# Performance work log

Hardware: AMD Instinct MI355X
Metric: run time of the kernel (lower is better)

The kernel has to match this reference:

```python
import jax, jax.numpy as jnp
import numpy as np

B, F, U, A, H = 8192, 1024, 256, 16, 8  # batch, in_features, units_layer, num_actions, hidden(=8)


def _coagent_layer(x, W0, b0, W1, b1, W2, b2):
    # x: [B, f_in]; stacked weights for U independent tiny MLPs (grouped GEMMs)
    h = jax.nn.relu(jnp.einsum('bf,uhf->buh', x, W0) + b0)   # [B, U, H]
    h = jax.nn.relu(jnp.einsum('buh,ugh->bug', h, W1) + b1)  # [B, U, H]
    q = jnp.einsum('bug,uag->bua', h, W2) + b2               # [B, U, A]
    # greedy action per coagent (epsilon-greedy with greedy=True / epsilon=0)
    return jnp.argmax(q, axis=-1).astype(jnp.float32)        # [B, U]


def setup_inputs() -> dict:
    key = jax.random.key(0)
    ks = jax.random.split(key, 19)
    n = lambda k, shape, fan: (jax.random.normal(k, shape, dtype=jnp.float32)
                               / jnp.sqrt(jnp.float32(fan)))
    return {
        'state': jax.random.normal(ks[0], (B, F), dtype=jnp.float32),
        # coagent layer 0: in_features -> 8 -> 8 -> A, stacked over U units
        'W0_0': n(ks[1], (U, H, F), F), 'b0_0': jnp.zeros((U, H), jnp.float32),
        'W1_0': n(ks[2], (U, H, H), H), 'b1_0': jnp.zeros((U, H), jnp.float32),
        'W2_0': n(ks[3], (U, A, H), H), 'b2_0': jnp.zeros((U, A), jnp.float32),
        # coagent layer 1: units_layer -> 8 -> 8 -> A, stacked over U units
        'W0_1': n(ks[4], (U, H, U), U), 'b0_1': jnp.zeros((U, H), jnp.float32),
        'W1_1': n(ks[5], (U, H, H), H), 'b1_1': jnp.zeros((U, H), jnp.float32),
        'W2_1': n(ks[6], (U, A, H), H), 'b2_1': jnp.zeros((U, A), jnp.float32),
        # Policy head: units_layer -> 8 -> 8 -> 1
        'PW0': n(ks[7], (H, U), U), 'Pb0': jnp.zeros((H,), jnp.float32),
        'PW1': n(ks[8], (H, H), H), 'Pb1': jnp.zeros((H,), jnp.float32),
        'PW2': n(ks[9], (1, H), H), 'Pb2': jnp.zeros((1,), jnp.float32),
    }


def reference(state, W0_0, b0_0, W1_0, b1_0, W2_0, b2_0,
              W0_1, b0_1, W1_1, b1_1, W2_1, b2_1,
              PW0, Pb0, PW1, Pb1, PW2, Pb2):
    a0 = _coagent_layer(state, W0_0, b0_0, W1_0, b1_0, W2_0, b2_0)  # [B, U]
    a1 = _coagent_layer(a0, W0_1, b0_1, W1_1, b1_1, W2_1, b2_1)     # [B, U]
    h = jax.nn.relu(a1 @ PW0.T + Pb0)
    h = jax.nn.relu(h @ PW1.T + Pb1)
    return h @ PW2.T + Pb2  # [B, 1]
```

## Files before the change

### kernel.cpp

```cpp
#include <hip/hip_runtime.h>
#include <cstring>
#include <cstdint>

#define B_TOTAL 8192
#define F_IN    1024
#define U_UNITS 256
#define NACT    16
#define HID     8

typedef float    f32x4  __attribute__((ext_vector_type(4)));
typedef _Float16 half8  __attribute__((ext_vector_type(8)));


__device__ __forceinline__ void gload_lds16(const _Float16* g, _Float16* l)
{
    __builtin_amdgcn_global_load_lds(
        (const __attribute__((address_space(1))) void*)g,
        (__attribute__((address_space(3))) void*)l,
        16, 0, 0);
}

__global__ __launch_bounds__(256)
void pack3_kernel(const float* __restrict__ s0, _Float16* __restrict__ d0h, _Float16* __restrict__ d0l,
                  const float* __restrict__ s1, _Float16* __restrict__ d1h, _Float16* __restrict__ d1l,
                  const float* __restrict__ s2, _Float16* __restrict__ d2h, _Float16* __restrict__ d2l)
{
    constexpr int NB0 = (B_TOTAL / 16) * (F_IN / 128);
    constexpr int NB1 = (U_UNITS * HID / 16) * (F_IN / 128);
    __shared__ float ls[16 * 132];
    int b = blockIdx.x;
    const float* src; _Float16 *dh, *dl; int K, lg;
    if (b < NB0)            { src = s0; dh = d0h; dl = d0l; K = F_IN;    lg = 3; }
    else if (b < NB0 + NB1) { b -= NB0; src = s1; dh = d1h; dl = d1l; K = F_IN; lg = 3; }
    else                    { b -= NB0 + NB1; src = s2; dh = d2h; dl = d2l; K = U_UNITS; lg = 1; }

    const int tid = threadIdx.x;
    const int mt  = b >> lg;
    const int kb  = b & ((1 << lg) - 1);
    const int r0  = mt * 16;

#pragma unroll
    for (int i = 0; i < 2; ++i) {
        const int e = tid + (i << 8);
        const int row = e >> 5;
        const int c4  = e & 31;
        f32x4 v = *reinterpret_cast<const f32x4*>(
            &src[(size_t)(r0 + row) * K + (kb << 7) + (c4 << 2)]);
        *reinterpret_cast<f32x4*>(&ls[row * 132 + (c4 << 2)]) = v;
    }
    __syncthreads();

    const int k8 = tid >> 4, r = tid & 15;
    float x[8];
#pragma unroll
    for (int j = 0; j < 8; ++j) x[j] = ls[r * 132 + (k8 << 3) + j];
    half8 h, l;
#pragma unroll
    for (int j = 0; j < 8; ++j) {
        h[j] = (_Float16)x[j];
        l[j] = (_Float16)((x[j] - (float)h[j]) * 2048.0f);
    }
    const size_t off = (((size_t)mt * (K >> 5)) + (kb << 2) + (k8 >> 2)) * 512
                     + (size_t)(((k8 & 3) << 4) + r) * 8;
    *reinterpret_cast<half8*>(&dh[off]) = h;
    *reinterpret_cast<half8*>(&dl[off]) = l;
}

constexpr int BM = 128, BN = 64;

template<int K_TOTAL, bool A_SPLIT, bool OUT_TF32>
__global__ __launch_bounds__(256, 4)
void coagent_mfma(const _Float16* __restrict__ Ahg, const _Float16* __restrict__ Alg,
                  const _Float16* __restrict__ Bhg, const _Float16* __restrict__ Blg,
                  const float* __restrict__ b0, const float* __restrict__ W1,
                  const float* __restrict__ b1, const float* __restrict__ W2,
                  const float* __restrict__ b2, void* __restrict__ outp)
{
    constexpr int BUFH  = A_SPLIT ? 12288 : 8192;
    constexpr int BOFFH = A_SPLIT ? 8192 : 4096;
    constexpr int BOFFL = A_SPLIT ? 10240 : 6144;
    constexpr int NCH   = A_SPLIT ? 6 : 4;

    struct EpiBufs { float Hs[BM][BN + 1]; _Float16 ab[BM * 8]; };
    union SMemU { _Float16 stage[2][BUFH]; EpiBufs epi; };
    __shared__ SMemU sm;

    constexpr int NTK = K_TOTAL >> 5;
    constexpr size_t TS = (size_t)NTK * 512;

    const int tid  = threadIdx.x;
    const int wave = tid >> 6;
    const int lane = tid & 63;
    const int quad = lane >> 4;
    const int l15  = lane & 15;

    const int flat = blockIdx.y * gridDim.x + blockIdx.x;
    const int xcd  = flat & 7;
    const int j    = flat >> 3;
    const int m0   = ((xcd << 3) | (j >> 5)) * BM;
    const int n0   = (j & 31) * BN;

    const int wmi = wave >> 1, wni = wave & 1;
    const int at  = wmi * 4;
    const int bt  = wni * 2;
    const int wm  = wmi * 64, wn = wni * 32;

    const int wave_u = __builtin_amdgcn_readfirstlane(wave);
    const _Float16* gs[NCH];
#pragma unroll
    for (int i = 0; i < NCH; ++i) {
        const int c = wave_u * NCH + i;
        const _Float16* base; int tile;
        if (A_SPLIT) {
            if (c < 8)       { base = Ahg; tile = (m0 >> 4) + c; }
            else if (c < 16) { base = Alg; tile = (m0 >> 4) + (c - 8); }
            else if (c < 20) { base = Bhg; tile = (n0 >> 4) + (c - 16); }
            else             { base = Blg; tile = (n0 >> 4) + (c - 20); }
        } else {
            if (c < 8)       { base = Ahg; tile = (m0 >> 4) + c; }
            else if (c < 12) { base = Bhg; tile = (n0 >> 4) + (c - 8); }
            else             { base = Blg; tile = (n0 >> 4) + (c - 12); }
        }
        gs[i] = base + (size_t)tile * TS;
    }
    const int loff = lane * 8;

    f32x4 acc1[4][2];
    f32x4 acc2[4][2];
#pragma unroll
    for (int i = 0; i < 4; ++i)
#pragma unroll
        for (int jj = 0; jj < 2; ++jj) { acc1[i][jj] = {0.f,0.f,0.f,0.f}; acc2[i][jj] = {0.f,0.f,0.f,0.f}; }

#pragma unroll
    for (int i = 0; i < NCH; ++i)
        gload_lds16(gs[i] + loff, &sm.stage[0][(wave_u * NCH + i) * 512]);
    __syncthreads();

    int cur = 0;
#pragma unroll 1
    for (int kt = 0; kt < NTK; ++kt) {
        if (kt + 1 < NTK) {
            _Float16* nb = &sm.stage[cur ^ 1][0];
#pragma unroll
            for (int i = 0; i < NCH; ++i)
                gload_lds16(gs[i] + (size_t)(kt + 1) * 512 + loff,
                            nb + (wave_u * NCH + i) * 512);
        }

        const _Float16* sb = &sm.stage[cur][0];
        half8 af[4], la[4];
#pragma unroll
        for (int mt = 0; mt < 4; ++mt)
            af[mt] = *reinterpret_cast<const half8*>(&sb[(at + mt) * 512 + lane * 8]);
        if constexpr (A_SPLIT) {
#pragma unroll
            for (int mt = 0; mt < 4; ++mt)
                la[mt] = *reinterpret_cast<const half8*>(&sb[4096 + (at + mt) * 512 + lane * 8]);
        }

#pragma unroll
        for (int nt = 0; nt < 2; ++nt) {
            half8 bf = *reinterpret_cast<const half8*>(&sb[BOFFH + (bt + nt) * 512 + lane * 8]);
            half8 lb = *reinterpret_cast<const half8*>(&sb[BOFFL + (bt + nt) * 512 + lane * 8]);
#pragma unroll
            for (int mt = 0; mt < 4; ++mt)
                acc1[mt][nt] = __builtin_amdgcn_mfma_f32_16x16x32_f16(af[mt], bf, acc1[mt][nt], 0, 0, 0);
            if constexpr (A_SPLIT) {
#pragma unroll
                for (int mt = 0; mt < 4; ++mt)
                    acc2[mt][nt] = __builtin_amdgcn_mfma_f32_16x16x32_f16(la[mt], bf, acc2[mt][nt], 0, 0, 0);
            }
#pragma unroll
            for (int mt = 0; mt < 4; ++mt)
                acc2[mt][nt] = __builtin_amdgcn_mfma_f32_16x16x32_f16(af[mt], lb, acc2[mt][nt], 0, 0, 0);
        }

        __syncthreads();
        cur ^= 1;
    }

#pragma unroll
    for (int mt = 0; mt < 4; ++mt)
#pragma unroll
        for (int nt = 0; nt < 2; ++nt)
#pragma unroll
            for (int r = 0; r < 4; ++r)
                sm.epi.Hs[wm + mt * 16 + quad * 4 + r][wn + nt * 16 + l15] =
                    acc1[mt][nt][r] + acc2[mt][nt][r] * (1.0f / 2048.0f);
    __syncthreads();

    const int ubase = n0 >> 3;
#pragma unroll
    for (int p = 0; p < 4; ++p) {
        const int idx = (p << 8) + tid;
        const int ul = idx >> 7;
        const int bl = idx & 127;
        const int u  = __builtin_amdgcn_readfirstlane(ubase + ul);
        const float* __restrict__ b0u = b0 + u * 8;
        const float* __restrict__ W1u = W1 + u * 64;
        const float* __restrict__ b1u = b1 + u * 8;
        const float* __restrict__ W2u = W2 + u * 128;
        const float* __restrict__ b2u = b2 + u * 16;

        float h[HID];
#pragma unroll
        for (int jj = 0; jj < HID; ++jj)
            h[jj] = fmaxf(sm.epi.Hs[bl][ul * 8 + jj] + b0u[jj], 0.f);

        float h2[HID];
#pragma unroll
        for (int g = 0; g < HID; ++g) {
            float s = b1u[g];
#pragma unroll
            for (int jj = 0; jj < HID; ++jj)
                s += h[jj] * W1u[g * 8 + jj];
            h2[g] = fmaxf(s, 0.f);
        }

        float best = b2u[0];
#pragma unroll
        for (int jj = 0; jj < HID; ++jj) best += h2[jj] * W2u[jj];
        int bi = 0;
#pragma unroll
        for (int a = 1; a < NACT; ++a) {
            float s = b2u[a];
#pragma unroll
            for (int jj = 0; jj < HID; ++jj)
                s += h2[jj] * W2u[a * 8 + jj];
            if (s > best) { best = s; bi = a; }
        }

        if (OUT_TF32) {
            ((float*)outp)[(size_t)u * B_TOTAL + m0 + bl] = (float)bi;
        } else {
            sm.epi.ab[bl * 8 + ul] = (_Float16)bi;
        }
    }
    if (!OUT_TF32) {
        __syncthreads();
        if (tid < 128) {
            float4 v = *reinterpret_cast<float4*>(&sm.epi.ab[tid * 8]);
            const int u = ubase;
            const int b = m0 + tid;
            const size_t off = ((size_t)(b >> 4) * 8 + (u >> 5)) * 512
                             + (size_t)((((u >> 3) & 3) << 4) + (b & 15)) * 8;
            *reinterpret_cast<float4*>(&((_Float16*)outp)[off]) = v;
        }
    }
}


constexpr int FBM = 128, FBN = 128, FBK = 16;

template<int K_TOTAL, bool X_TRANSPOSED>
__global__ __launch_bounds__(256, 2)
void coagent_kernel(const float* __restrict__ X, const float* __restrict__ W0,
                    const float* __restrict__ b0, const float* __restrict__ W1,
                    const float* __restrict__ b1, const float* __restrict__ W2,
                    const float* __restrict__ b2, float* __restrict__ outT)
{
    struct SMemGemm { float As[FBK][FBM + 4]; float Bs[FBK][FBN + 4]; };
    union SMem { SMemGemm g; float Hs[FBM][65]; };
    __shared__ SMem sm;

    const int tid = threadIdx.x;
    const int tx = tid & 15, ty = tid >> 4;
    const int m0 = blockIdx.y * FBM, n0 = blockIdx.x * FBN;

    float acc[8][8];
#pragma unroll
    for (int i = 0; i < 8; ++i)
#pragma unroll
        for (int j = 0; j < 8; ++j) acc[i][j] = 0.f;

    for (int k0 = 0; k0 < K_TOTAL; k0 += FBK) {
        __syncthreads();
        if (X_TRANSPOSED) {
#pragma unroll
            for (int l = tid; l < (FBM * FBK) / 4; l += 256) {
                const int k = l >> 5, q = l & 31;
                const float4 v = *reinterpret_cast<const float4*>(
                    &X[(size_t)(k0 + k) * B_TOTAL + m0 + 4 * q]);
                *reinterpret_cast<float4*>(&sm.g.As[k][4 * q]) = v;
            }
        } else {
#pragma unroll
            for (int l = tid; l < (FBM * FBK) / 4; l += 256) {
                const int row = l >> 2, c = l & 3;
                const float4 v = *reinterpret_cast<const float4*>(
                    &X[(size_t)(m0 + row) * K_TOTAL + k0 + 4 * c]);
                sm.g.As[4 * c + 0][row] = v.x; sm.g.As[4 * c + 1][row] = v.y;
                sm.g.As[4 * c + 2][row] = v.z; sm.g.As[4 * c + 3][row] = v.w;
            }
        }
#pragma unroll
        for (int l = tid; l < (FBN * FBK) / 4; l += 256) {
            const int row = l >> 2, c = l & 3;
            const float4 v = *reinterpret_cast<const float4*>(
                &W0[(size_t)(n0 + row) * K_TOTAL + k0 + 4 * c]);
            sm.g.Bs[4 * c + 0][row] = v.x; sm.g.Bs[4 * c + 1][row] = v.y;
            sm.g.Bs[4 * c + 2][row] = v.z; sm.g.Bs[4 * c + 3][row] = v.w;
        }
        __syncthreads();
#pragma unroll
        for (int k = 0; k < FBK; ++k) {
            float a[8], bb[8];
            *reinterpret_cast<float4*>(&a[0])  = *reinterpret_cast<float4*>(&sm.g.As[k][4 * ty]);
            *reinterpret_cast<float4*>(&a[4])  = *reinterpret_cast<float4*>(&sm.g.As[k][64 + 4 * ty]);
            *reinterpret_cast<float4*>(&bb[0]) = *reinterpret_cast<float4*>(&sm.g.Bs[k][4 * tx]);
            *reinterpret_cast<float4*>(&bb[4]) = *reinterpret_cast<float4*>(&sm.g.Bs[k][64 + 4 * tx]);
#pragma unroll
            for (int i = 0; i < 8; ++i)
#pragma unroll
                for (int j = 0; j < 8; ++j) acc[i][j] += a[i] * bb[j];
        }
    }

    const int ub_base = n0 >> 3;
    for (int half = 0; half < 2; ++half) {
        __syncthreads();
#pragma unroll
        for (int i = 0; i < 8; ++i) {
            const int row = (i < 4) ? (4 * ty + i) : (64 + 4 * ty + (i - 4));
#pragma unroll
            for (int j = 0; j < 4; ++j)
                sm.Hs[row][4 * tx + j] = acc[i][4 * half + j];
        }
        __syncthreads();
#pragma unroll
        for (int p = 0; p < 4; ++p) {
            const int pair = (p << 8) + tid;
            const int ul = pair >> 7, bl = pair & 127;
            const int u = ub_base + half * 8 + ul;
            float h[HID];
#pragma unroll
            for (int j = 0; j < HID; ++j)
                h[j] = fmaxf(sm.Hs[bl][ul * 8 + j] + b0[u * 8 + j], 0.f);
            float h2[HID];
#pragma unroll
            for (int g = 0; g < HID; ++g) {
                float s = b1[u * 8 + g];
#pragma unroll
                for (int j = 0; j < HID; ++j) s += h[j] * W1[u * 64 + g * 8 + j];
                h2[g] = fmaxf(s, 0.f);
            }
            float best = b2[u * 16];
#pragma unroll
            for (int j = 0; j < HID; ++j) best += h2[j] * W2[u * 128 + j];
            int bi = 0;
#pragma unroll
            for (int a = 1; a < NACT; ++a) {
                float s = b2[u * 16 + a];
#pragma unroll
                for (int j = 0; j < HID; ++j) s += h2[j] * W2[u * 128 + a * 8 + j];
                if (s > best) { best = s; bi = a; }
            }
            outT[(size_t)u * B_TOTAL + m0 + bl] = (float)bi;
        }
    }
}

__global__ __launch_bounds__(256)
void policy_kernel(const float* __restrict__ A1T,
                   const float* __restrict__ PW0, const float* __restrict__ Pb0,
                   const float* __restrict__ PW1, const float* __restrict__ Pb1,
                   const float* __restrict__ PW2, const float* __restrict__ Pb2,
                   float* __restrict__ out)
{
    __shared__ float part[8][32][HID + 1];
    const int tid = threadIdx.x;
    const int b32 = tid & 31;
    const int sl  = tid >> 5;
    const int b   = blockIdx.x * 32 + b32;

    float hp[HID];
#pragma unroll
    for (int j = 0; j < HID; ++j) hp[j] = 0.f;

#pragma unroll 1
    for (int q0 = 0; q0 < 32; q0 += 8) {
        float v[8];
#pragma unroll
        for (int t = 0; t < 8; ++t)
            v[t] = A1T[(size_t)(sl * 32 + q0 + t) * B_TOTAL + b];
#pragma unroll
        for (int t = 0; t < 8; ++t)
#pragma unroll
            for (int j = 0; j < HID; ++j)
                hp[j] += v[t] * PW0[j * U_UNITS + sl * 32 + q0 + t];
    }
#pragma unroll
    for (int j = 0; j < HID; ++j) part[sl][b32][j] = hp[j];
    __syncthreads();

    if (sl == 0) {
        float h[HID];
#pragma unroll
        for (int j = 0; j < HID; ++j) {
            float s = Pb0[j];
#pragma unroll
            for (int s8 = 0; s8 < 8; ++s8) s += part[s8][b32][j];
            h[j] = fmaxf(s, 0.f);
        }
        float h2[HID];
#pragma unroll
        for (int g = 0; g < HID; ++g) {
            float s = Pb1[g];
#pragma unroll
            for (int j = 0; j < HID; ++j) s += h[j] * PW1[g * 8 + j];
            h2[g] = fmaxf(s, 0.f);
        }
        float o = Pb2[0];
#pragma unroll
        for (int j = 0; j < HID; ++j) o += h2[j] * PW2[j];
        out[b] = o;
    }
}


extern "C" void kernel_launch(void* const* d_in, const int* in_sizes, int n_in,
                              void* d_out, int out_size, void* d_ws, size_t ws_size,
                              hipStream_t stream)
{
    const float* state = (const float*)d_in[0];
    const float* W0_0  = (const float*)d_in[1];
    const float* b0_0  = (const float*)d_in[2];
    const float* W1_0  = (const float*)d_in[3];
    const float* b1_0  = (const float*)d_in[4];
    const float* W2_0  = (const float*)d_in[5];
    const float* b2_0  = (const float*)d_in[6];
    const float* W0_1  = (const float*)d_in[7];
    const float* b0_1  = (const float*)d_in[8];
    const float* W1_1  = (const float*)d_in[9];
    const float* b1_1  = (const float*)d_in[10];
    const float* W2_1  = (const float*)d_in[11];
    const float* b2_1  = (const float*)d_in[12];
    const float* PW0   = (const float*)d_in[13];
    const float* Pb0   = (const float*)d_in[14];
    const float* PW1   = (const float*)d_in[15];
    const float* Pb1   = (const float*)d_in[16];
    const float* PW2   = (const float*)d_in[17];
    const float* Pb2   = (const float*)d_in[18];

    const size_t SZ_STATE = (size_t)B_TOTAL * F_IN;
    const size_t SZ_W00   = (size_t)U_UNITS * HID * F_IN;
    const size_t SZ_W01   = (size_t)U_UNITS * HID * U_UNITS;
    const size_t NEED = (2 * SZ_STATE + 2 * SZ_W00 + 2 * SZ_W01
                         + (size_t)B_TOTAL * U_UNITS) * 2
                        + (size_t)U_UNITS * B_TOTAL * 4;

    if (ws_size >= NEED) {
        char* p = (char*)d_ws;
        _Float16* state_h = (_Float16*)p;                p += SZ_STATE * 2;
        _Float16* state_l = (_Float16*)p;                p += SZ_STATE * 2;
        _Float16* w00_h   = (_Float16*)p;                p += SZ_W00 * 2;
        _Float16* w00_l   = (_Float16*)p;                p += SZ_W00 * 2;
        _Float16* w01_h   = (_Float16*)p;                p += SZ_W01 * 2;
        _Float16* w01_l   = (_Float16*)p;                p += SZ_W01 * 2;
        _Float16* a0      = (_Float16*)p;                p += (size_t)B_TOTAL * U_UNITS * 2;
        float*    a1T     = (float*)p;

        constexpr int NB0 = (B_TOTAL / 16) * (F_IN / 128);
        constexpr int NB1 = (U_UNITS * HID / 16) * (F_IN / 128);
        constexpr int NB2 = (U_UNITS * HID / 16) * (U_UNITS / 128);
        pack3_kernel<<<NB0 + NB1 + NB2, 256, 0, stream>>>(
            state, state_h, state_l, W0_0, w00_h, w00_l, W0_1, w01_h, w01_l);

        dim3 grid((U_UNITS * HID) / BN, B_TOTAL / BM);

        coagent_mfma<F_IN, true, false><<<grid, 256, 0, stream>>>(
            state_h, state_l, w00_h, w00_l, b0_0, W1_0, b1_0, W2_0, b2_0, (void*)a0);

        coagent_mfma<U_UNITS, false, true><<<grid, 256, 0, stream>>>(
            a0, nullptr, w01_h, w01_l, b0_1, W1_1, b1_1, W2_1, b2_1, (void*)a1T);

        policy_kernel<<<B_TOTAL / 32, 256, 0, stream>>>(
            a1T, PW0, Pb0, PW1, Pb1, PW2, Pb2, (float*)d_out);
    } else {
        float* a0T = (float*)d_ws;
        float* a1T = a0T + (size_t)U_UNITS * B_TOTAL;
        dim3 grid((U_UNITS * HID) / FBN, B_TOTAL / FBM);
        coagent_kernel<F_IN, false><<<grid, 256, 0, stream>>>(
            state, W0_0, b0_0, W1_0, b1_0, W2_0, b2_0, a0T);
        coagent_kernel<U_UNITS, true><<<grid, 256, 0, stream>>>(
            a0T, W0_1, b0_1, W1_1, b1_1, W2_1, b2_1, a1T);
        policy_kernel<<<B_TOTAL / 32, 256, 0, stream>>>(
            a1T, PW0, Pb0, PW1, Pb1, PW2, Pb2, (float*)d_out);
    }
}
```

Before: 297.0 us.

## Widen MFMA coagent tile to 128x128 with 8 waves and split epilogue

Doubles the N tile of the MFMA coagent GEMMs from 64 to 128 columns and moves to 512-thread blocks with 8 waves arranged 2x4. This halves the number of times the A (state) tiles are re-read across the grid. The epilogue now runs in two halves so the existing shared-memory Hs buffer can be reused. The XCD-aware block swizzle is removed, blocks are mapped directly from blockIdx, and the inner loop now keeps B fragments in registers while streaming A. The larger block and shared-memory footprint may lower occupancy, and the extra epilogue syncs add serialization.

Result: faster. 267.6 us (median of 2 runs) (-9.9%).

```diff
diff --git a/kernel.cpp b/kernel.cpp
--- a/kernel.cpp
+++ b/kernel.cpp
@@ -66,22 +66,22 @@
     *reinterpret_cast<half8*>(&dl[off]) = l;
 }
 
-constexpr int BM = 128, BN = 64;
+constexpr int BM = 128, BN = 128;
 
 template<int K_TOTAL, bool A_SPLIT, bool OUT_TF32>
-__global__ __launch_bounds__(256, 4)
+__global__ __launch_bounds__(512, 4)
 void coagent_mfma(const _Float16* __restrict__ Ahg, const _Float16* __restrict__ Alg,
                   const _Float16* __restrict__ Bhg, const _Float16* __restrict__ Blg,
                   const float* __restrict__ b0, const float* __restrict__ W1,
                   const float* __restrict__ b1, const float* __restrict__ W2,
                   const float* __restrict__ b2, void* __restrict__ outp)
 {
-    constexpr int BUFH  = A_SPLIT ? 12288 : 8192;
+    constexpr int BUFH  = A_SPLIT ? 16384 : 12288;
     constexpr int BOFFH = A_SPLIT ? 8192 : 4096;
-    constexpr int BOFFL = A_SPLIT ? 10240 : 6144;
-    constexpr int NCH   = A_SPLIT ? 6 : 4;
-
-    struct EpiBufs { float Hs[BM][BN + 1]; _Float16 ab[BM * 8]; };
+    constexpr int BOFFL = A_SPLIT ? 12288 : 8192;
+    constexpr int NCH   = A_SPLIT ? 4 : 3;
+
+    struct EpiBufs { float Hs[BM][65]; _Float16 ab[BM * 8]; };
     union SMemU { _Float16 stage[2][BUFH]; EpiBufs epi; };
     __shared__ SMemU sm;
 
@@ -94,16 +94,14 @@
     const int quad = lane >> 4;
     const int l15  = lane & 15;
 
-    const int flat = blockIdx.y * gridDim.x + blockIdx.x;
-    const int xcd  = flat & 7;
-    const int j    = flat >> 3;
-    const int m0   = ((xcd << 3) | (j >> 5)) * BM;
-    const int n0   = (j & 31) * BN;
-
-    const int wmi = wave >> 1, wni = wave & 1;
+    const int m0 = blockIdx.y * BM;
+    const int n0 = blockIdx.x * BN;
+
+    const int wmi = wave >> 2;
+    const int wni = wave & 3;
     const int at  = wmi * 4;
     const int bt  = wni * 2;
-    const int wm  = wmi * 64, wn = wni * 32;
+    const int wm  = wmi * 64;
 
     const int wave_u = __builtin_amdgcn_readfirstlane(wave);
     const _Float16* gs[NCH];
@@ -114,12 +112,12 @@
         if (A_SPLIT) {
             if (c < 8)       { base = Ahg; tile = (m0 >> 4) + c; }
             else if (c < 16) { base = Alg; tile = (m0 >> 4) + (c - 8); }
-            else if (c < 20) { base = Bhg; tile = (n0 >> 4) + (c - 16); }
-            else             { base = Blg; tile = (n0 >> 4) + (c - 20); }
+            else if (c < 24) { base = Bhg; tile = (n0 >> 4) + (c - 16); }
+            else             { base = Blg; tile = (n0 >> 4) + (c - 24); }
         } else {
             if (c < 8)       { base = Ahg; tile = (m0 >> 4) + c; }
-            else if (c < 12) { base = Bhg; tile = (n0 >> 4) + (c - 8); }
-            else             { base = Blg; tile = (n0 >> 4) + (c - 12); }
+            else if (c < 16) { base = Bhg; tile = (n0 >> 4) + (c - 8); }
+            else             { base = Blg; tile = (n0 >> 4) + (c - 16); }
         }
         gs[i] = base + (size_t)tile * TS;
     }
@@ -149,103 +147,103 @@
         }
 
         const _Float16* sb = &sm.stage[cur][0];
-        half8 af[4], la[4];
-#pragma unroll
-        for (int mt = 0; mt < 4; ++mt)
-            af[mt] = *reinterpret_cast<const half8*>(&sb[(at + mt) * 512 + lane * 8]);
-        if constexpr (A_SPLIT) {
+        half8 bf[2], lb[2];
+#pragma unroll
+        for (int nt = 0; nt < 2; ++nt) {
+            bf[nt] = *reinterpret_cast<const half8*>(&sb[BOFFH + (bt + nt) * 512 + lane * 8]);
+            lb[nt] = *reinterpret_cast<const half8*>(&sb[BOFFL + (bt + nt) * 512 + lane * 8]);
+        }
+#pragma unroll
+        for (int mt = 0; mt < 4; ++mt) {
+            half8 af = *reinterpret_cast<const half8*>(&sb[(at + mt) * 512 + lane * 8]);
+#pragma unroll
+            for (int nt = 0; nt < 2; ++nt)
+                acc1[mt][nt] = __builtin_amdgcn_mfma_f32_16x16x32_f16(af, bf[nt], acc1[mt][nt], 0, 0, 0);
+            if constexpr (A_SPLIT) {
+                half8 la = *reinterpret_cast<const half8*>(&sb[4096 + (at + mt) * 512 + lane * 8]);
+#pragma unroll
+                for (int nt = 0; nt < 2; ++nt)
+                    acc2[mt][nt] = __builtin_amdgcn_mfma_f32_16x16x32_f16(la, bf[nt], acc2[mt][nt], 0, 0, 0);
+            }
+#pragma unroll
+            for (int nt = 0; nt < 2; ++nt)
+                acc2[mt][nt] = __builtin_amdgcn_mfma_f32_16x16x32_f16(af, lb[nt], acc2[mt][nt], 0, 0, 0);
+        }
+
+        __syncthreads();
+        cur ^= 1;
+    }
+
+    const int ubase = n0 >> 3;
+    for (int half = 0; half < 2; ++half) {
+        __syncthreads();
+        if ((wni >> 1) == half) {
 #pragma unroll
             for (int mt = 0; mt < 4; ++mt)
-                la[mt] = *reinterpret_cast<const half8*>(&sb[4096 + (at + mt) * 512 + lane * 8]);
-        }
-
-#pragma unroll
-        for (int nt = 0; nt < 2; ++nt) {
-            half8 bf = *reinterpret_cast<const half8*>(&sb[BOFFH + (bt + nt) * 512 + lane * 8]);
-            half8 lb = *reinterpret_cast<const half8*>(&sb[BOFFL + (bt + nt) * 512 + lane * 8]);
-#pragma unroll
-            for (int mt = 0; mt < 4; ++mt)
-                acc1[mt][nt] = __builtin_amdgcn_mfma_f32_16x16x32_f16(af[mt], bf, acc1[mt][nt], 0, 0, 0);
-            if constexpr (A_SPLIT) {
-#pragma unroll
-                for (int mt = 0; mt < 4; ++mt)
-                    acc2[mt][nt] = __builtin_amdgcn_mfma_f32_16x16x32_f16(la[mt], bf, acc2[mt][nt], 0, 0, 0);
-            }
-#pragma unroll
-            for (int mt = 0; mt < 4; ++mt)
-                acc2[mt][nt] = __builtin_amdgcn_mfma_f32_16x16x32_f16(af[mt], lb, acc2[mt][nt], 0, 0, 0);
-        }
-
-        __syncthreads();
-        cur ^= 1;
-    }
-
-#pragma unroll
-    for (int mt = 0; mt < 4; ++mt)
-#pragma unroll
-        for (int nt = 0; nt < 2; ++nt)
-#pragma unroll
-            for (int r = 0; r < 4; ++r)
-                sm.epi.Hs[wm + mt * 16 + quad * 4 + r][wn + nt * 16 + l15] =
-                    acc1[mt][nt][r] + acc2[mt][nt][r] * (1.0f / 2048.0f);
-    __syncthreads();
-
-    const int ubase = n0 >> 3;
-#pragma unroll
-    for (int p = 0; p < 4; ++p) {
-        const int idx = (p << 8) + tid;
-        const int ul = idx >> 7;
-        const int bl = idx & 127;
-        const int u  = __builtin_amdgcn_readfirstlane(ubase + ul);
-        const float* __restrict__ b0u = b0 + u * 8;
-        const float* __restrict__ W1u = W1 + u * 64;
-        const float* __restrict__ b1u = b1 + u * 8;
-        const float* __restrict__ W2u = W2 + u * 128;
-        const float* __restrict__ b2u = b2 + u * 16;
-
-        float h[HID];
-#pragma unroll
-        for (int jj = 0; jj < HID; ++jj)
-            h[jj] = fmaxf(sm.epi.Hs[bl][ul * 8 + jj] + b0u[jj], 0.f);
-
-        float h2[HID];
-#pragma unroll
-        for (int g = 0; g < HID; ++g) {
-            float s = b1u[g];
+#pragma unroll
+                for (int nt = 0; nt < 2; ++nt)
+#pragma unroll
+                    for (int r = 0; r < 4; ++r)
+                        sm.epi.Hs[wm + mt * 16 + quad * 4 + r][(wni & 1) * 32 + nt * 16 + l15] =
+                            acc1[mt][nt][r] + acc2[mt][nt][r] * (1.0f / 2048.0f);
+        }
+        __syncthreads();
+#pragma unroll
+        for (int p = 0; p < 2; ++p) {
+            const int idx = (p << 9) + tid;
+            const int ul = idx >> 7;
+            const int bl = idx & 127;
+            const int u  = __builtin_amdgcn_readfirstlane(ubase + half * 8 + ul);
+            const float* __restrict__ b0u = b0 + u * 8;
+            const float* __restrict__ W1u = W1 + u * 64;
+            const float* __restrict__ b1u = b1 + u * 8;
+            const float* __restrict__ W2u = W2 + u * 128;
+            const float* __restrict__ b2u = b2 + u * 16;
+
+            float h[HID];
 #pragma unroll
             for (int jj = 0; jj < HID; ++jj)
-                s += h[jj] * W1u[g * 8 + jj];
-            h2[g] = fmaxf(s, 0.f);
-        }
-
-        float best = b2u[0];
-#pragma unroll
-        for (int jj = 0; jj < HID; ++jj) best += h2[jj] * W2u[jj];
-        int bi = 0;
-#pragma unroll
-        for (int a = 1; a < NACT; ++a) {
-            float s = b2u[a];
-#pragma unroll
-            for (int jj = 0; jj < HID; ++jj)
-                s += h2[jj] * W2u[a * 8 + jj];
-            if (s > best) { best = s; bi = a; }
-        }
-
-        if (OUT_TF32) {
-            ((float*)outp)[(size_t)u * B_TOTAL + m0 + bl] = (float)bi;
-        } else {
-            sm.epi.ab[bl * 8 + ul] = (_Float16)bi;
-        }
-    }
-    if (!OUT_TF32) {
-        __syncthreads();
-        if (tid < 128) {
-            float4 v = *reinterpret_cast<float4*>(&sm.epi.ab[tid * 8]);
-            const int u = ubase;
-            const int b = m0 + tid;
-            const size_t off = ((size_t)(b >> 4) * 8 + (u >> 5)) * 512
-                             + (size_t)((((u >> 3) & 3) << 4) + (b & 15)) * 8;
-            *reinterpret_cast<float4*>(&((_Float16*)outp)[off]) = v;
+                h[jj] = fmaxf(sm.epi.Hs[bl][ul * 8 + jj] + b0u[jj], 0.f);
+
+            float h2[HID];
+#pragma unroll
+            for (int g = 0; g < HID; ++g) {
+                float s = b1u[g];
+#pragma unroll
+                for (int jj = 0; jj < HID; ++jj)
+                    s += h[jj] * W1u[g * 8 + jj];
+                h2[g] = fmaxf(s, 0.f);
+            }
+
+            float best = b2u[0];
+#pragma unroll
+            for (int jj = 0; jj < HID; ++jj) best += h2[jj] * W2u[jj];
+            int bi = 0;
+#pragma unroll
+            for (int a = 1; a < NACT; ++a) {
+                float s = b2u[a];
+#pragma unroll
+                for (int jj = 0; jj < HID; ++jj)
+                    s += h2[jj] * W2u[a * 8 + jj];
+                if (s > best) { best = s; bi = a; }
+            }
+
+            if (OUT_TF32) {
+                ((float*)outp)[(size_t)u * B_TOTAL + m0 + bl] = (float)bi;
+            } else {
+                sm.epi.ab[bl * 8 + ul] = (_Float16)bi;
+            }
+        }
+        if (!OUT_TF32) {
+            __syncthreads();
+            if (tid < 128) {
+                float4 v = *reinterpret_cast<float4*>(&sm.epi.ab[tid * 8]);
+                const int u = ubase + half * 8;
+                const int b = m0 + tid;
+                const size_t off = ((size_t)(b >> 4) * 8 + (u >> 5)) * 512
+                                 + (size_t)((((u >> 3) & 3) << 4) + (b & 15)) * 8;
+                *reinterpret_cast<float4*>(&((_Float16*)outp)[off]) = v;
+            }
         }
     }
 }
@@ -469,10 +467,10 @@
 
         dim3 grid((U_UNITS * HID) / BN, B_TOTAL / BM);
 
-        coagent_mfma<F_IN, true, false><<<grid, 256, 0, stream>>>(
+        coagent_mfma<F_IN, true, false><<<grid, 512, 0, stream>>>(
             state_h, state_l, w00_h, w00_l, b0_0, W1_0, b1_0, W2_0, b2_0, (void*)a0);
 
-        coagent_mfma<U_UNITS, false, true><<<grid, 256, 0, stream>>>(
+        coagent_mfma<U_UNITS, false, true><<<grid, 512, 0, stream>>>(
             a0, nullptr, w01_h, w01_l, b0_1, W1_1, b1_1, W2_1, b2_1, (void*)a1T);
 
         policy_kernel<<<B_TOTAL / 32, 256, 0, stream>>>(
```
